# Optimization experiments

Measured on AMD Instinct MI355X. Metric: run time of the kernel, lower is better.

Reference implementation:

```python
import jax, jax.numpy as jnp
import numpy as np

T, B, L = 40, 64, 80
D_IN = 256
H = 4 * D_IN  # 1024
A = 18


def _lstm_scan(x, h0, c0, W_ih, W_hh, b_ih, b_hh):
    # x: [S,B,in] -> outputs [S,B,H]; PyTorch gate order i,f,g,o
    b = b_ih + b_hh
    def step(carry, xt):
        h, c = carry
        g = xt @ W_ih.T + h @ W_hh.T + b
        i, f, gg, o = jnp.split(g, 4, axis=-1)
        c = jax.nn.sigmoid(f) * c + jax.nn.sigmoid(i) * jnp.tanh(gg)
        h = jax.nn.sigmoid(o) * jnp.tanh(c)
        return (h, c), h
    (h, c), ys = jax.lax.scan(step, (h0, c0), x)
    return ys, h, c


def setup_inputs() -> dict:
    key = jax.random.key(0)
    ks = jax.random.split(key, 24)
    def rn(k, shape, scale=0.02):
        return jax.random.normal(k, shape, dtype=jnp.float32) * scale
    return {
        "state": rn(ks[0], (T, B, D_IN), 1.0),
        "demonstration": rn(ks[1], (T, B, L, D_IN), 1.0),
        "demonstration_length": jax.random.randint(ks[2], (T, B), 1, L + 1, dtype=jnp.int32),
        "h0": jnp.zeros((B, H), jnp.float32),
        "c0": jnp.zeros((B, H), jnp.float32),
        "enc_Wih": rn(ks[3], (4 * H, D_IN)),
        "enc_Whh": rn(ks[4], (4 * H, H)),
        "enc_bih": rn(ks[5], (4 * H,)),
        "enc_bhh": rn(ks[6], (4 * H,)),
        "attn_W": rn(ks[7], (1, 2 * H)),
        "attn_b": rn(ks[8], (1,)),
        "comb_W": rn(ks[9], (H, H + D_IN)),
        "comb_b": rn(ks[10], (H,)),
        "lstm_Wih": rn(ks[11], (4 * H, H)),
        "lstm_Whh": rn(ks[12], (4 * H, H)),
        "lstm_bih": rn(ks[13], (4 * H,)),
        "lstm_bhh": rn(ks[14], (4 * H,)),
        "mid_W": rn(ks[15], (H, H)),
        "mid_b": rn(ks[16], (H,)),
        "out_W": rn(ks[17], (A, H)),
        "out_b": rn(ks[18], (A,)),
    }


def reference(state, demonstration, demonstration_length, h0, c0,
              enc_Wih, enc_Whh, enc_bih, enc_bhh,
              attn_W, attn_b, comb_W, comb_b,
              lstm_Wih, lstm_Whh, lstm_bih, lstm_bhh,
              mid_W, mid_b, out_W, out_b):
    lengths = demonstration_length[0]              # [B], only t=0 lengths used (as in original)
    demo0 = demonstration[0]                       # [B,L,D_IN], only t=0 demo used
    z = jnp.zeros((B, H), demo0.dtype)
    enc, _, _ = _lstm_scan(demo0.transpose(1, 0, 2), z, z,
                           enc_Wih, enc_Whh, enc_bih, enc_bhh)  # [L,B,H]
    enc = enc.transpose(1, 0, 2)                   # [B,L,H]
    mask = jnp.arange(L)[None, :] < lengths[:, None]  # [B,L]
    # attn(cat(enc, h)) == enc @ Wd^T + h @ Wh^T + b (split of the concat linear)
    Wd, Wh = attn_W[:, :H], attn_W[:, H:]          # [1,H] each
    score_d = (enc @ Wd.T)[..., 0] + attn_b[0]     # [B,L], constant over t
    lstm_b = lstm_bih + lstm_bhh

    def step(carry, obs_t):
        h, c = carry
        scores = score_d + h @ Wh.T                # [B,L] ([B,1] broadcast)
        scores = jnp.where(mask, scores, -jnp.inf)
        w = jax.nn.softmax(scores, axis=-1)        # masked softmax over demo steps
        attn_applied = jnp.einsum('bl,blh->bh', w, enc)
        x = jax.nn.relu(jnp.concatenate([attn_applied, obs_t], axis=-1) @ comb_W.T + comb_b)
        g = x @ lstm_Wih.T + h @ lstm_Whh.T + lstm_b
        i, f, gg, o = jnp.split(g, 4, axis=-1)
        c = jax.nn.sigmoid(f) * c + jax.nn.sigmoid(i) * jnp.tanh(gg)
        h = jax.nn.sigmoid(o) * jnp.tanh(c)
        m = h @ mid_W.T + mid_b                    # no activation between middle and output (as in source)
        q_t = m @ out_W.T + out_b
        return (h, c), q_t

    (h, c), q = jax.lax.scan(step, (h0, c0), state)  # q: [T,B,A]
    return q, h, c
```

## Files before the change

kernel.cpp:

```cpp
#include <hip/hip_runtime.h>
#include <hip/hip_bf16.h>

#define TT 40
#define BB 64
#define LL 80
#define DD 256
#define HH 1024
#define G4H 4096
#define AA 18
#define KENC 1280
#define KLSTM 2048
#define KCOMB 1280
#define QSZ (TT*BB*AA)

typedef __bf16 bf16x8 __attribute__((ext_vector_type(8)));
typedef float  f32x4  __attribute__((ext_vector_type(4)));

#define OFF_WENC   ((size_t)0)
#define OFF_WLSTM  (OFF_WENC  + (size_t)G4H*KENC*2)
#define OFF_WCOMB  (OFF_WLSTM + (size_t)G4H*KLSTM*2)
#define OFF_WMID   (OFF_WCOMB + (size_t)HH*KCOMB*2)
#define OFF_BIASE  (OFF_WMID  + (size_t)HH*HH*2)
#define OFF_BIASL  (OFF_BIASE + (size_t)G4H*4)
#define OFF_DEMO   (OFF_BIASL + (size_t)G4H*4)
#define OFF_STATE  (OFF_DEMO  + (size_t)BB*LL*DD*2)
#define OFF_ENC    (OFF_STATE + (size_t)TT*BB*DD*2)
#define OFF_HDEC   (OFF_ENC   + (size_t)BB*LL*HH*2)
#define OFF_XALL   (OFF_HDEC  + (size_t)TT*BB*HH*2)
#define OFF_MF     (OFF_XALL  + (size_t)TT*BB*HH*2)
#define OFF_ATTNS  (OFF_MF    + (size_t)TT*BB*HH*2)
#define OFF_CF     (OFF_ATTNS + (size_t)BB*HH*2)
#define OFF_HBUF   (OFF_CF    + (size_t)BB*HH*4)

__device__ __forceinline__ float sigm(float x){ return 1.f/(1.f+__expf(-x)); }

__device__ __forceinline__ float wred_sum(float v){
#pragma unroll
  for (int s=32; s>0; s>>=1) v += __shfl_xor(v, s, 64);
  return v;
}
__device__ __forceinline__ float wred_max(float v){
#pragma unroll
  for (int s=32; s>0; s>>=1) v = fmaxf(v, __shfl_xor(v, s, 64));
  return v;
}
__device__ __forceinline__ unsigned pack_bf16(float a, float b){
  unsigned short ua = __builtin_bit_cast(unsigned short, (__bf16)a);
  unsigned short ub = __builtin_bit_cast(unsigned short, (__bf16)b);
  return (unsigned)ua | ((unsigned)ub << 16);
}

__global__ void k_pack_enc(const float* __restrict__ wih, const float* __restrict__ whh,
                           const float* __restrict__ bih, const float* __restrict__ bhh,
                           __bf16* __restrict__ dst, float* __restrict__ bias){
  int p = blockIdx.x;
  int gate = p & 3, jj = (p >> 2) & 3, bq = p >> 4;
  int orig = gate*HH + bq*4 + jj;
  if (threadIdx.x == 0) bias[p] = bih[orig] + bhh[orig];
  const float* s0 = wih + (size_t)orig*DD;
  const float* s1 = whh + (size_t)orig*HH;
  __bf16* d = dst + (size_t)p*KENC;
  for (int k = threadIdx.x; k < KENC; k += blockDim.x)
    d[k] = (__bf16)(k < DD ? s0[k] : s1[k-DD]);
}
__global__ void k_pack_lstm(const float* __restrict__ wih, const float* __restrict__ whh,
                            const float* __restrict__ bih, const float* __restrict__ bhh,
                            __bf16* __restrict__ dst, float* __restrict__ bias){
  int p = blockIdx.x;
  int gate = p & 3, jj = (p >> 2) & 3, bq = p >> 4;
  int orig = gate*HH + bq*4 + jj;
  if (threadIdx.x == 0) bias[p] = bih[orig] + bhh[orig];
  const float* s0 = wih + (size_t)orig*HH;
  const float* s1 = whh + (size_t)orig*HH;
  __bf16* d = dst + (size_t)p*KLSTM;
  for (int k = threadIdx.x; k < KLSTM; k += blockDim.x)
    d[k] = (__bf16)(k < HH ? s0[k] : s1[k-HH]);
}
__global__ void k_conv(const float* __restrict__ src, __bf16* __restrict__ dst, int n){
  int i = blockIdx.x*blockDim.x + threadIdx.x;
  if (i < n) dst[i] = (__bf16)src[i];
}

__global__ __launch_bounds__(256)
void k_enc_step(const __bf16* __restrict__ demoC, const __bf16* __restrict__ wEnc,
                const float* __restrict__ bE, const __bf16* __restrict__ hR,
                __bf16* __restrict__ hW, __bf16* __restrict__ encB,
                float* __restrict__ cf, int t){
  const int bk = blockIdx.x, tid = threadIdx.x;
  const int wv = tid >> 6, ln = tid & 63;
  const int l15 = ln & 15, lhi = ln >> 4;
  const int klane = lhi * 8;
  const int am = wv*16 + l15;

  __shared__ float g_lds[BB*17];

  const __bf16* brow = wEnc + (size_t)(bk*16 + l15)*KENC;
  const __bf16* arow = demoC + ((size_t)am*LL + t)*DD;
  const __bf16* hrow = hR + (size_t)am*HH;

  f32x4 acc = {0.f,0.f,0.f,0.f};
#pragma unroll 8
  for (int kk = 0; kk < KENC; kk += 32) {
    int k0 = kk + klane;
    const __bf16* pa = (k0 < DD) ? (arow + k0) : (hrow + (k0 - DD));
    acc = __builtin_amdgcn_mfma_f32_16x16x32_bf16(*(const bf16x8*)pa,
                                                  *(const bf16x8*)(brow + k0), acc, 0,0,0);
  }
  {
    int r0 = wv*16 + lhi*4;
#pragma unroll
    for (int r = 0; r < 4; ++r) g_lds[(r0+r)*17 + l15] = acc[r];
  }
  __syncthreads();
  if (tid < 128) {
    const int m_ = tid >> 1, q2 = tid & 1;
    const int j0_ = bk*4 + 2*q2;
    int gb = m_*17 + q2*8, cb = bk*16 + q2*8;
    float gi0 = g_lds[gb+0]+bE[cb+0], gf0 = g_lds[gb+1]+bE[cb+1];
    float gg0 = g_lds[gb+2]+bE[cb+2], go0 = g_lds[gb+3]+bE[cb+3];
    float gi1 = g_lds[gb+4]+bE[cb+4], gf1 = g_lds[gb+5]+bE[cb+5];
    float gg1 = g_lds[gb+6]+bE[cb+6], go1 = g_lds[gb+7]+bE[cb+7];
    float cA = cf[m_*HH + j0_], cB = cf[m_*HH + j0_ + 1];
    float cn0 = sigm(gf0)*cA + sigm(gi0)*tanhf(gg0);
    float cn1 = sigm(gf1)*cB + sigm(gi1)*tanhf(gg1);
    float hn0 = sigm(go0)*tanhf(cn0);
    float hn1 = sigm(go1)*tanhf(cn1);
    cf[m_*HH + j0_] = cn0; cf[m_*HH + j0_ + 1] = cn1;
    unsigned hp = pack_bf16(hn0, hn1);
    *(unsigned*)(hW + (size_t)m_*HH + j0_) = hp;
    *(unsigned*)(encB + ((size_t)m_*LL + t)*HH + j0_) = hp;
  }
}

__global__ __launch_bounds__(512)
void k_dec_step(const __bf16* __restrict__ xall, const __bf16* __restrict__ wLstm,
                const float* __restrict__ bL, const __bf16* __restrict__ hR,
                __bf16* __restrict__ hW, __bf16* __restrict__ hdec,
                float* __restrict__ cf, float* __restrict__ out, int t){
  const int bk = blockIdx.x, tid = threadIdx.x;
  const int wv = tid >> 6, ln = tid & 63;
  const int l15 = ln & 15, lhi = ln >> 4;
  const int klane = lhi * 8;
  const int mt = wv & 3;
  const int am = mt*16 + l15;
  const int khalf = wv >> 2;

  __shared__ float g_lds [BB*17];
  __shared__ float g_lds2[BB*17];

  const __bf16* brow = wLstm + (size_t)(bk*16 + l15)*KLSTM + khalf*HH;
  const __bf16* arow = khalf ? (hR + (size_t)am*HH)
                             : (xall + ((size_t)t*BB + am)*HH);

  f32x4 acc = {0.f,0.f,0.f,0.f};
#pragma unroll 8
  for (int kk = 0; kk < HH; kk += 32) {
    int k0 = kk + klane;
    acc = __builtin_amdgcn_mfma_f32_16x16x32_bf16(*(const bf16x8*)(arow + k0),
                                                  *(const bf16x8*)(brow + k0), acc, 0,0,0);
  }
  {
    float* gl = khalf ? g_lds2 : g_lds;
    int r0 = mt*16 + lhi*4;
#pragma unroll
    for (int r = 0; r < 4; ++r) gl[(r0+r)*17 + l15] = acc[r];
  }
  __syncthreads();
  if (tid < 128) {
    const int m_ = tid >> 1, q2 = tid & 1;
    const int j0_ = bk*4 + 2*q2;
    int gb = m_*17 + q2*8, cb = bk*16 + q2*8;
    float gi0 = g_lds[gb+0]+g_lds2[gb+0]+bL[cb+0], gf0 = g_lds[gb+1]+g_lds2[gb+1]+bL[cb+1];
    float gg0 = g_lds[gb+2]+g_lds2[gb+2]+bL[cb+2], go0 = g_lds[gb+3]+g_lds2[gb+3]+bL[cb+3];
    float gi1 = g_lds[gb+4]+g_lds2[gb+4]+bL[cb+4], gf1 = g_lds[gb+5]+g_lds2[gb+5]+bL[cb+5];
    float gg1 = g_lds[gb+6]+g_lds2[gb+6]+bL[cb+6], go1 = g_lds[gb+7]+g_lds2[gb+7]+bL[cb+7];
    float cA = cf[m_*HH + j0_], cB = cf[m_*HH + j0_ + 1];
    float cn0 = sigm(gf0)*cA + sigm(gi0)*tanhf(gg0);
    float cn1 = sigm(gf1)*cB + sigm(gi1)*tanhf(gg1);
    float hn0 = sigm(go0)*tanhf(cn0);
    float hn1 = sigm(go1)*tanhf(cn1);
    cf[m_*HH + j0_] = cn0; cf[m_*HH + j0_ + 1] = cn1;
    unsigned hp = pack_bf16(hn0, hn1);
    *(unsigned*)(hW + (size_t)m_*HH + j0_) = hp;
    *(unsigned*)(hdec + ((size_t)t*BB + m_)*HH + j0_) = hp;
    if (t == TT-1) {
      out[QSZ + m_*HH + j0_]     = hn0;
      out[QSZ + m_*HH + j0_ + 1] = hn1;
    }
  }
}

__global__ __launch_bounds__(256)
void k_attn(const int* __restrict__ demlen, const float* __restrict__ h0,
            const float* __restrict__ c0, const float* __restrict__ attn_w,
            const __bf16* __restrict__ encB, __bf16* __restrict__ attnS,
            __bf16* __restrict__ hD0, float* __restrict__ cf){
  const int bk = blockIdx.x, tid = threadIdx.x;
  const int wv = tid >> 6, ln = tid & 63;
  __shared__ float sc_sh[LL];
  __shared__ float w_sh[LL];
  int b = bk >> 2, qq = bk & 3;
  for (int i = 0; i < 20; ++i) {
    int l = wv*20 + i;
    const __bf16* er = encB + ((size_t)b*LL + l)*HH + ln*16;
    bf16x8 e0 = *(const bf16x8*)(er);
    bf16x8 e1 = *(const bf16x8*)(er + 8);
    float part = 0.f;
#pragma unroll
    for (int j = 0; j < 8; ++j) {
      part += (float)e0[j] * attn_w[ln*16 + j];
      part += (float)e1[j] * attn_w[ln*16 + 8 + j];
    }
    part = wred_sum(part);
    if (ln == 0) sc_sh[l] = part;
  }
  __syncthreads();
  if (wv == 0) {
    int len = demlen[b];
    float s0 = (ln < len) ? sc_sh[ln] : -1e30f;
    float s1 = (ln < 16 && 64+ln < len) ? sc_sh[64+ln] : -1e30f;
    float mx = wred_max(fmaxf(s0, s1));
    float e0 = __expf(s0 - mx);
    float e1 = (ln < 16) ? __expf(s1 - mx) : 0.f;
    float inv = 1.f / wred_sum(e0 + e1);
    w_sh[ln] = e0 * inv;
    if (ln < 16) w_sh[64+ln] = e1 * inv;
  }
  __syncthreads();
  {
    int col = qq*256 + tid;
    float a = 0.f;
    const __bf16* eb = encB + (size_t)b*LL*HH + col;
#pragma unroll 4
    for (int l = 0; l < LL; ++l) a += w_sh[l] * (float)eb[(size_t)l*HH];
    attnS[(size_t)b*HH + col] = (__bf16)a;
  }
  int gtid = bk*256 + tid;
  for (int i = gtid; i < BB*HH/2; i += 256*256) {
    int i2 = i*2;
    *((unsigned*)hD0 + i) = pack_bf16(h0[i2], h0[i2+1]);
  }
  for (int i = gtid; i < BB*HH; i += 256*256) cf[i] = c0[i];
}

__global__ __launch_bounds__(256)
void k_x(const __bf16* __restrict__ attnS, const __bf16* __restrict__ stateB,
         const __bf16* __restrict__ wComb, const float* __restrict__ comb_b,
         __bf16* __restrict__ xall){
  const int bk = blockIdx.x, tid = threadIdx.x;
  const int wv = tid >> 6, ln = tid & 63;
  const int l15 = ln & 15, lhi = ln >> 4;
  const int klane = lhi * 8;
  int g = bk*4 + wv;
  for (int i = 0; i < 10; ++i) {
    int ti = i*1024 + g;
    int mtt = ti >> 6, nt = ti & 63;
    f32x4 acc = {0.f,0.f,0.f,0.f};
    const __bf16* brow = wComb + (size_t)(nt*16 + l15)*KCOMB;
    int r = mtt*16 + l15, bb = r & 63;
    const __bf16* aat = attnS + (size_t)bb*HH;
    const __bf16* ast = stateB + (size_t)r*DD;
#pragma unroll 8
    for (int kk = 0; kk < KCOMB; kk += 32) {
      int k0 = kk + klane;
      bf16x8 af = (k0 < HH) ? *(const bf16x8*)(aat + k0)
                            : *(const bf16x8*)(ast + (k0-HH));
      acc = __builtin_amdgcn_mfma_f32_16x16x32_bf16(af, *(const bf16x8*)(brow + k0), acc, 0,0,0);
    }
    int col = nt*16 + l15;
    float cb = comb_b[col];
    int r0 = mtt*16 + lhi*4;
#pragma unroll
    for (int rr = 0; rr < 4; ++rr)
      xall[(size_t)(r0+rr)*HH + col] = (__bf16)fmaxf(acc[rr]+cb, 0.f);
  }
}

__global__ __launch_bounds__(256)
void k_mid(const __bf16* __restrict__ hdec, const __bf16* __restrict__ wMid,
           const float* __restrict__ mid_b, __bf16* __restrict__ mf){
  const int bk = blockIdx.x, tid = threadIdx.x;
  const int wv = tid >> 6, ln = tid & 63;
  const int l15 = ln & 15, lhi = ln >> 4;
  const int klane = lhi * 8;
  int g = bk*4 + wv;
  for (int i = 0; i < 10; ++i) {
    int ti = i*1024 + g;
    int mtt = ti >> 6, nt = ti & 63;
    f32x4 acc = {0.f,0.f,0.f,0.f};
    const __bf16* brow = wMid + (size_t)(nt*16 + l15)*HH;
    const __bf16* arow = hdec + (size_t)(mtt*16 + l15)*HH;
#pragma unroll 8
    for (int kk = 0; kk < HH; kk += 32) {
      int k0 = kk + klane;
      acc = __builtin_amdgcn_mfma_f32_16x16x32_bf16(*(const bf16x8*)(arow + k0),
                                                    *(const bf16x8*)(brow + k0), acc, 0,0,0);
    }
    int col = nt*16 + l15;
    float mb = mid_b[col];
    int r0 = mtt*16 + lhi*4;
#pragma unroll
    for (int rr = 0; rr < 4; ++rr)
      mf[(size_t)(r0+rr)*HH + col] = (__bf16)(acc[rr]+mb);
  }
}

__global__ __launch_bounds__(256)
void k_out(const __bf16* __restrict__ mf, const float* __restrict__ out_w,
           const float* __restrict__ out_b, float* __restrict__ out){
  const int bk = blockIdx.x, tid = threadIdx.x;
  const int wv = tid >> 6, ln = tid & 63;
  int g = bk*4 + wv;
  for (int i = 0; i < 3; ++i) {
    int row = i*1024 + g;
    if (row < TT*BB) {
      const __bf16* mr = mf + (size_t)row*HH;
      float mreg[16];
#pragma unroll
      for (int k = 0; k < 16; ++k) mreg[k] = (float)mr[ln + 64*k];
      for (int a = 0; a < AA; ++a) {
        float p = 0.f;
#pragma unroll
        for (int k = 0; k < 16; ++k) p += mreg[k] * out_w[(size_t)a*HH + ln + 64*k];
        p = wred_sum(p);
        if (ln == 0) out[(size_t)row*AA + a] = p + out_b[a];
      }
    }
  }
}

__global__ void k_fin(const float* __restrict__ cf, float* __restrict__ out){
  int i = blockIdx.x*blockDim.x + threadIdx.x;
  if (i < BB*HH) out[QSZ + BB*HH + i] = cf[i];
}

extern "C" void kernel_launch(void* const* d_in, const int* in_sizes, int n_in,
                              void* d_out, int out_size, void* d_ws, size_t ws_size,
                              hipStream_t stream) {
  (void)in_sizes; (void)n_in; (void)out_size; (void)ws_size;
  const float* state    = (const float*)d_in[0];
  const float* demo     = (const float*)d_in[1];
  const int*   demlen   = (const int*)d_in[2];
  const float* h0       = (const float*)d_in[3];
  const float* c0       = (const float*)d_in[4];
  const float* enc_wih  = (const float*)d_in[5];
  const float* enc_whh  = (const float*)d_in[6];
  const float* enc_bih  = (const float*)d_in[7];
  const float* enc_bhh  = (const float*)d_in[8];
  const float* attn_w   = (const float*)d_in[9];
  const float* comb_w   = (const float*)d_in[11];
  const float* comb_b   = (const float*)d_in[12];
  const float* lstm_wih = (const float*)d_in[13];
  const float* lstm_whh = (const float*)d_in[14];
  const float* lstm_bih = (const float*)d_in[15];
  const float* lstm_bhh = (const float*)d_in[16];
  const float* mid_w    = (const float*)d_in[17];
  const float* mid_b    = (const float*)d_in[18];
  const float* out_w    = (const float*)d_in[19];
  const float* out_b    = (const float*)d_in[20];
  char* ws = (char*)d_ws;

  __bf16* wEnc  = (__bf16*)(ws + OFF_WENC);
  __bf16* wLstm = (__bf16*)(ws + OFF_WLSTM);
  __bf16* wComb = (__bf16*)(ws + OFF_WCOMB);
  __bf16* wMid  = (__bf16*)(ws + OFF_WMID);
  float*  bE    = (float*)(ws + OFF_BIASE);
  float*  bL    = (float*)(ws + OFF_BIASL);
  __bf16* demoC = (__bf16*)(ws + OFF_DEMO);
  __bf16* stateB= (__bf16*)(ws + OFF_STATE);
  __bf16* encB  = (__bf16*)(ws + OFF_ENC);
  __bf16* hdec  = (__bf16*)(ws + OFF_HDEC);
  __bf16* xall  = (__bf16*)(ws + OFF_XALL);
  __bf16* mf    = (__bf16*)(ws + OFF_MF);
  __bf16* attnS = (__bf16*)(ws + OFF_ATTNS);
  float*  cf    = (float*)(ws + OFF_CF);
  __bf16* hbE0  = (__bf16*)(ws + OFF_HBUF);
  __bf16* hbE1  = hbE0 + (size_t)BB*HH;
  __bf16* hbD0  = hbE1 + (size_t)BB*HH;
  __bf16* hbD1  = hbD0 + (size_t)BB*HH;
  float*  out   = (float*)d_out;

  (void)hipMemsetAsync(cf,   0, (size_t)BB*HH*4, stream);
  (void)hipMemsetAsync(hbE0, 0, (size_t)BB*HH*2, stream);
  k_pack_enc <<<G4H, 256, 0, stream>>>(enc_wih, enc_whh, enc_bih, enc_bhh, wEnc, bE);
  k_pack_lstm<<<G4H, 256, 0, stream>>>(lstm_wih, lstm_whh, lstm_bih, lstm_bhh, wLstm, bL);
  k_conv<<<(HH*KCOMB + 255)/256, 256, 0, stream>>>(comb_w, wComb, HH*KCOMB);
  k_conv<<<(HH*HH   + 255)/256, 256, 0, stream>>>(mid_w,  wMid,  HH*HH);
  k_conv<<<(BB*LL*DD + 255)/256, 256, 0, stream>>>(demo,  demoC,  BB*LL*DD);
  k_conv<<<(TT*BB*DD + 255)/256, 256, 0, stream>>>(state, stateB, TT*BB*DD);

  for (int t = 0; t < LL; ++t) {
    __bf16* hR = (t & 1) ? hbE1 : hbE0;
    __bf16* hW = (t & 1) ? hbE0 : hbE1;
    k_enc_step<<<256, 256, 0, stream>>>(demoC, wEnc, bE, hR, hW, encB, cf, t);
  }
  k_attn<<<256, 256, 0, stream>>>(demlen, h0, c0, attn_w, encB, attnS, hbD0, cf);
  k_x<<<256, 256, 0, stream>>>(attnS, stateB, wComb, comb_b, xall);
  for (int t = 0; t < TT; ++t) {
    __bf16* hR = (t & 1) ? hbD1 : hbD0;
    __bf16* hW = (t & 1) ? hbD0 : hbD1;
    k_dec_step<<<256, 512, 0, stream>>>(xall, wLstm, bL, hR, hW, hdec, cf, out, t);
  }
  k_mid<<<256, 256, 0, stream>>>(hdec, wMid, mid_b, mf);
  k_out<<<256, 256, 0, stream>>>(mf, out_w, out_b, out);
  k_fin<<<(BB*HH + 255)/256, 256, 0, stream>>>(cf, out);
}
```

Before: 1.915 ms.

## Split-K recurrent steps across 16 waves and merge prep kernels into one launch

The encoder and decoder per-step kernels now run 1024 threads per block and split the K reduction four ways across waves, reducing the partial sums through LDS. This shortens each wave's serial MFMA chain on the latency-bound recurrence. All weight packing, conversions and memsets are merged into a single prep kernel, and the final c-state copy is folded into k_out, cutting launch count. The cost is more LDS traffic per step and a larger block size, which can limit occupancy.

```diff
diff --git a/kernel.cpp b/kernel.cpp
--- a/kernel.cpp
+++ b/kernel.cpp
@@ -50,38 +50,65 @@
   return (unsigned)ua | ((unsigned)ub << 16);
 }
 
-__global__ void k_pack_enc(const float* __restrict__ wih, const float* __restrict__ whh,
-                           const float* __restrict__ bih, const float* __restrict__ bhh,
-                           __bf16* __restrict__ dst, float* __restrict__ bias){
-  int p = blockIdx.x;
-  int gate = p & 3, jj = (p >> 2) & 3, bq = p >> 4;
-  int orig = gate*HH + bq*4 + jj;
-  if (threadIdx.x == 0) bias[p] = bih[orig] + bhh[orig];
-  const float* s0 = wih + (size_t)orig*DD;
-  const float* s1 = whh + (size_t)orig*HH;
-  __bf16* d = dst + (size_t)p*KENC;
-  for (int k = threadIdx.x; k < KENC; k += blockDim.x)
-    d[k] = (__bf16)(k < DD ? s0[k] : s1[k-DD]);
-}
-__global__ void k_pack_lstm(const float* __restrict__ wih, const float* __restrict__ whh,
-                            const float* __restrict__ bih, const float* __restrict__ bhh,
-                            __bf16* __restrict__ dst, float* __restrict__ bias){
-  int p = blockIdx.x;
-  int gate = p & 3, jj = (p >> 2) & 3, bq = p >> 4;
-  int orig = gate*HH + bq*4 + jj;
-  if (threadIdx.x == 0) bias[p] = bih[orig] + bhh[orig];
-  const float* s0 = wih + (size_t)orig*HH;
-  const float* s1 = whh + (size_t)orig*HH;
-  __bf16* d = dst + (size_t)p*KLSTM;
-  for (int k = threadIdx.x; k < KLSTM; k += blockDim.x)
-    d[k] = (__bf16)(k < HH ? s0[k] : s1[k-HH]);
-}
-__global__ void k_conv(const float* __restrict__ src, __bf16* __restrict__ dst, int n){
-  int i = blockIdx.x*blockDim.x + threadIdx.x;
-  if (i < n) dst[i] = (__bf16)src[i];
-}
-
+#define PB1 4096
+#define PB2 8192
+#define PB3 13312
+#define PB4 17408
+#define PB5 22528
+#define PB6 25088
+#define PB7 25344
+#define PGRID 25472
 __global__ __launch_bounds__(256)
+void k_prep(const float* __restrict__ enc_wih, const float* __restrict__ enc_whh,
+            const float* __restrict__ enc_bih, const float* __restrict__ enc_bhh,
+            const float* __restrict__ lstm_wih, const float* __restrict__ lstm_whh,
+            const float* __restrict__ lstm_bih, const float* __restrict__ lstm_bhh,
+            const float* __restrict__ comb_w, const float* __restrict__ mid_w,
+            const float* __restrict__ demo, const float* __restrict__ state,
+            char* __restrict__ ws){
+  int blk = blockIdx.x, tid = threadIdx.x;
+  if (blk < PB1) {
+    int p = blk;
+    int gate = p & 3, jj = (p >> 2) & 3, bq = p >> 4;
+    int orig = gate*HH + bq*4 + jj;
+    if (tid == 0) ((float*)(ws + OFF_BIASE))[p] = enc_bih[orig] + enc_bhh[orig];
+    const float* s0 = enc_wih + (size_t)orig*DD;
+    const float* s1 = enc_whh + (size_t)orig*HH;
+    __bf16* d = (__bf16*)(ws + OFF_WENC) + (size_t)p*KENC;
+    for (int k = tid; k < KENC; k += 256)
+      d[k] = (__bf16)(k < DD ? s0[k] : s1[k-DD]);
+  } else if (blk < PB2) {
+    int p = blk - PB1;
+    int gate = p & 3, jj = (p >> 2) & 3, bq = p >> 4;
+    int orig = gate*HH + bq*4 + jj;
+    if (tid == 0) ((float*)(ws + OFF_BIASL))[p] = lstm_bih[orig] + lstm_bhh[orig];
+    const float* s0 = lstm_wih + (size_t)orig*HH;
+    const float* s1 = lstm_whh + (size_t)orig*HH;
+    __bf16* d = (__bf16*)(ws + OFF_WLSTM) + (size_t)p*KLSTM;
+    for (int k = tid; k < KLSTM; k += 256)
+      d[k] = (__bf16)(k < HH ? s0[k] : s1[k-HH]);
+  } else if (blk < PB3) {
+    int i = (blk - PB2)*256 + tid;
+    ((__bf16*)(ws + OFF_WCOMB))[i] = (__bf16)comb_w[i];
+  } else if (blk < PB4) {
+    int i = (blk - PB3)*256 + tid;
+    ((__bf16*)(ws + OFF_WMID))[i] = (__bf16)mid_w[i];
+  } else if (blk < PB5) {
+    int i = (blk - PB4)*256 + tid;
+    ((__bf16*)(ws + OFF_DEMO))[i] = (__bf16)demo[i];
+  } else if (blk < PB6) {
+    int i = (blk - PB5)*256 + tid;
+    ((__bf16*)(ws + OFF_STATE))[i] = (__bf16)state[i];
+  } else if (blk < PB7) {
+    int i = (blk - PB6)*256 + tid;
+    ((float*)(ws + OFF_CF))[i] = 0.f;
+  } else {
+    int i = (blk - PB7)*256 + tid;
+    ((unsigned*)(ws + OFF_HBUF))[i] = 0u;
+  }
+}
+
+__global__ __launch_bounds__(1024)
 void k_enc_step(const __bf16* __restrict__ demoC, const __bf16* __restrict__ wEnc,
                 const float* __restrict__ bE, const __bf16* __restrict__ hR,
                 __bf16* __restrict__ hW, __bf16* __restrict__ encB,
@@ -90,41 +117,43 @@
   const int wv = tid >> 6, ln = tid & 63;
   const int l15 = ln & 15, lhi = ln >> 4;
   const int klane = lhi * 8;
-  const int am = wv*16 + l15;
-
-  __shared__ float g_lds[BB*17];
+  const int mt = wv & 3, kq = wv >> 2;
+  const int am = mt*16 + l15;
+
+  __shared__ float g_lds[4][BB*17];
 
   const __bf16* brow = wEnc + (size_t)(bk*16 + l15)*KENC;
   const __bf16* arow = demoC + ((size_t)am*LL + t)*DD;
   const __bf16* hrow = hR + (size_t)am*HH;
 
   f32x4 acc = {0.f,0.f,0.f,0.f};
-#pragma unroll 8
-  for (int kk = 0; kk < KENC; kk += 32) {
-    int k0 = kk + klane;
+  const int kb = kq*320;
+#pragma unroll
+  for (int kk = 0; kk < 320; kk += 32) {
+    int k0 = kb + kk + klane;
     const __bf16* pa = (k0 < DD) ? (arow + k0) : (hrow + (k0 - DD));
     acc = __builtin_amdgcn_mfma_f32_16x16x32_bf16(*(const bf16x8*)pa,
                                                   *(const bf16x8*)(brow + k0), acc, 0,0,0);
   }
   {
-    int r0 = wv*16 + lhi*4;
-#pragma unroll
-    for (int r = 0; r < 4; ++r) g_lds[(r0+r)*17 + l15] = acc[r];
+    int r0 = mt*16 + lhi*4;
+#pragma unroll
+    for (int r = 0; r < 4; ++r) g_lds[kq][(r0+r)*17 + l15] = acc[r];
   }
   __syncthreads();
   if (tid < 128) {
     const int m_ = tid >> 1, q2 = tid & 1;
     const int j0_ = bk*4 + 2*q2;
     int gb = m_*17 + q2*8, cb = bk*16 + q2*8;
-    float gi0 = g_lds[gb+0]+bE[cb+0], gf0 = g_lds[gb+1]+bE[cb+1];
-    float gg0 = g_lds[gb+2]+bE[cb+2], go0 = g_lds[gb+3]+bE[cb+3];
-    float gi1 = g_lds[gb+4]+bE[cb+4], gf1 = g_lds[gb+5]+bE[cb+5];
-    float gg1 = g_lds[gb+6]+bE[cb+6], go1 = g_lds[gb+7]+bE[cb+7];
+    float g[8];
+#pragma unroll
+    for (int j = 0; j < 8; ++j)
+      g[j] = g_lds[0][gb+j] + g_lds[1][gb+j] + g_lds[2][gb+j] + g_lds[3][gb+j] + bE[cb+j];
     float cA = cf[m_*HH + j0_], cB = cf[m_*HH + j0_ + 1];
-    float cn0 = sigm(gf0)*cA + sigm(gi0)*tanhf(gg0);
-    float cn1 = sigm(gf1)*cB + sigm(gi1)*tanhf(gg1);
-    float hn0 = sigm(go0)*tanhf(cn0);
-    float hn1 = sigm(go1)*tanhf(cn1);
+    float cn0 = sigm(g[1])*cA + sigm(g[0])*tanhf(g[2]);
+    float cn1 = sigm(g[5])*cB + sigm(g[4])*tanhf(g[6]);
+    float hn0 = sigm(g[3])*tanhf(cn0);
+    float hn1 = sigm(g[7])*tanhf(cn1);
     cf[m_*HH + j0_] = cn0; cf[m_*HH + j0_ + 1] = cn1;
     unsigned hp = pack_bf16(hn0, hn1);
     *(unsigned*)(hW + (size_t)m_*HH + j0_) = hp;
@@ -132,7 +161,7 @@
   }
 }
 
-__global__ __launch_bounds__(512)
+__global__ __launch_bounds__(1024)
 void k_dec_step(const __bf16* __restrict__ xall, const __bf16* __restrict__ wLstm,
                 const float* __restrict__ bL, const __bf16* __restrict__ hR,
                 __bf16* __restrict__ hW, __bf16* __restrict__ hdec,
@@ -141,44 +170,41 @@
   const int wv = tid >> 6, ln = tid & 63;
   const int l15 = ln & 15, lhi = ln >> 4;
   const int klane = lhi * 8;
-  const int mt = wv & 3;
+  const int mt = wv & 3, kq = wv >> 2;
   const int am = mt*16 + l15;
-  const int khalf = wv >> 2;
-
-  __shared__ float g_lds [BB*17];
-  __shared__ float g_lds2[BB*17];
-
-  const __bf16* brow = wLstm + (size_t)(bk*16 + l15)*KLSTM + khalf*HH;
-  const __bf16* arow = khalf ? (hR + (size_t)am*HH)
-                             : (xall + ((size_t)t*BB + am)*HH);
+
+  __shared__ float g_lds[4][BB*17];
+
+  const __bf16* brow = wLstm + (size_t)(bk*16 + l15)*KLSTM + kq*512;
+  const __bf16* arow = (kq < 2) ? (xall + ((size_t)t*BB + am)*HH + kq*512)
+                                : (hR + (size_t)am*HH + (kq-2)*512);
 
   f32x4 acc = {0.f,0.f,0.f,0.f};
-#pragma unroll 8
-  for (int kk = 0; kk < HH; kk += 32) {
+#pragma unroll
+  for (int kk = 0; kk < 512; kk += 32) {
     int k0 = kk + klane;
     acc = __builtin_amdgcn_mfma_f32_16x16x32_bf16(*(const bf16x8*)(arow + k0),
                                                   *(const bf16x8*)(brow + k0), acc, 0,0,0);
   }
   {
-    float* gl = khalf ? g_lds2 : g_lds;
     int r0 = mt*16 + lhi*4;
 #pragma unroll
-    for (int r = 0; r < 4; ++r) gl[(r0+r)*17 + l15] = acc[r];
+    for (int r = 0; r < 4; ++r) g_lds[kq][(r0+r)*17 + l15] = acc[r];
   }
   __syncthreads();
   if (tid < 128) {
     const int m_ = tid >> 1, q2 = tid & 1;
     const int j0_ = bk*4 + 2*q2;
     int gb = m_*17 + q2*8, cb = bk*16 + q2*8;
-    float gi0 = g_lds[gb+0]+g_lds2[gb+0]+bL[cb+0], gf0 = g_lds[gb+1]+g_lds2[gb+1]+bL[cb+1];
-    float gg0 = g_lds[gb+2]+g_lds2[gb+2]+bL[cb+2], go0 = g_lds[gb+3]+g_lds2[gb+3]+bL[cb+3];
-    float gi1 = g_lds[gb+4]+g_lds2[gb+4]+bL[cb+4], gf1 = g_lds[gb+5]+g_lds2[gb+5]+bL[cb+5];
-    float gg1 = g_lds[gb+6]+g_lds2[gb+6]+bL[cb+6], go1 = g_lds[gb+7]+g_lds2[gb+7]+bL[cb+7];
+    float g[8];
+#pragma unroll
+    for (int j = 0; j < 8; ++j)
+      g[j] = g_lds[0][gb+j] + g_lds[1][gb+j] + g_lds[2][gb+j] + g_lds[3][gb+j] + bL[cb+j];
     float cA = cf[m_*HH + j0_], cB = cf[m_*HH + j0_ + 1];
-    float cn0 = sigm(gf0)*cA + sigm(gi0)*tanhf(gg0);
-    float cn1 = sigm(gf1)*cB + sigm(gi1)*tanhf(gg1);
-    float hn0 = sigm(go0)*tanhf(cn0);
-    float hn1 = sigm(go1)*tanhf(cn1);
+    float cn0 = sigm(g[1])*cA + sigm(g[0])*tanhf(g[2]);
+    float cn1 = sigm(g[5])*cB + sigm(g[4])*tanhf(g[6]);
+    float hn0 = sigm(g[3])*tanhf(cn0);
+    float hn1 = sigm(g[7])*tanhf(cn1);
     cf[m_*HH + j0_] = cn0; cf[m_*HH + j0_ + 1] = cn1;
     unsigned hp = pack_bf16(hn0, hn1);
     *(unsigned*)(hW + (size_t)m_*HH + j0_) = hp;
@@ -307,7 +333,8 @@
 
 __global__ __launch_bounds__(256)
 void k_out(const __bf16* __restrict__ mf, const float* __restrict__ out_w,
-           const float* __restrict__ out_b, float* __restrict__ out){
+           const float* __restrict__ out_b, const float* __restrict__ cf,
+           float* __restrict__ out){
   const int bk = blockIdx.x, tid = threadIdx.x;
   const int wv = tid >> 6, ln = tid & 63;
   int g = bk*4 + wv;
@@ -327,11 +354,8 @@
       }
     }
   }
-}
-
-__global__ void k_fin(const float* __restrict__ cf, float* __restrict__ out){
-  int i = blockIdx.x*blockDim.x + threadIdx.x;
-  if (i < BB*HH) out[QSZ + BB*HH + i] = cf[i];
+  for (int i = bk*256 + tid; i < BB*HH; i += 256*256)
+    out[QSZ + BB*HH + i] = cf[i];
 }
 
 extern "C" void kernel_launch(void* const* d_in, const int* in_sizes, int n_in,
@@ -380,28 +404,21 @@
   __bf16* hbD1  = hbD0 + (size_t)BB*HH;
   float*  out   = (float*)d_out;
 
-  (void)hipMemsetAsync(cf,   0, (size_t)BB*HH*4, stream);
-  (void)hipMemsetAsync(hbE0, 0, (size_t)BB*HH*2, stream);
-  k_pack_enc <<<G4H, 256, 0, stream>>>(enc_wih, enc_whh, enc_bih, enc_bhh, wEnc, bE);
-  k_pack_lstm<<<G4H, 256, 0, stream>>>(lstm_wih, lstm_whh, lstm_bih, lstm_bhh, wLstm, bL);
-  k_conv<<<(HH*KCOMB + 255)/256, 256, 0, stream>>>(comb_w, wComb, HH*KCOMB);
-  k_conv<<<(HH*HH   + 255)/256, 256, 0, stream>>>(mid_w,  wMid,  HH*HH);
-  k_conv<<<(BB*LL*DD + 255)/256, 256, 0, stream>>>(demo,  demoC,  BB*LL*DD);
-  k_conv<<<(TT*BB*DD + 255)/256, 256, 0, stream>>>(state, stateB, TT*BB*DD);
-
+  k_prep<<<PGRID, 256, 0, stream>>>(enc_wih, enc_whh, enc_bih, enc_bhh,
+                                    lstm_wih, lstm_whh, lstm_bih, lstm_bhh,
+                                    comb_w, mid_w, demo, state, ws);
   for (int t = 0; t < LL; ++t) {
     __bf16* hR = (t & 1) ? hbE1 : hbE0;
     __bf16* hW = (t & 1) ? hbE0 : hbE1;
-    k_enc_step<<<256, 256, 0, stream>>>(demoC, wEnc, bE, hR, hW, encB, cf, t);
+    k_enc_step<<<256, 1024, 0, stream>>>(demoC, wEnc, bE, hR, hW, encB, cf, t);
   }
   k_attn<<<256, 256, 0, stream>>>(demlen, h0, c0, attn_w, encB, attnS, hbD0, cf);
   k_x<<<256, 256, 0, stream>>>(attnS, stateB, wComb, comb_b, xall);
   for (int t = 0; t < TT; ++t) {
     __bf16* hR = (t & 1) ? hbD1 : hbD0;
     __bf16* hW = (t & 1) ? hbD0 : hbD1;
-    k_dec_step<<<256, 512, 0, stream>>>(xall, wLstm, bL, hR, hW, hdec, cf, out, t);
+    k_dec_step<<<256, 1024, 0, stream>>>(xall, wLstm, bL, hR, hW, hdec, cf, out, t);
   }
   k_mid<<<256, 256, 0, stream>>>(hdec, wMid, mid_b, mf);
-  k_out<<<256, 256, 0, stream>>>(mf, out_w, out_b, out);
-  k_fin<<<(BB*HH + 255)/256, 256, 0, stream>>>(cf, out);
-}
+  k_out<<<256, 256, 0, stream>>>(mf, out_w, out_b, cf, out);
+}
```

New measurement: 1.910 ms, median of 2. About the same (-0.3%).
